# Kernel optimization log

Hardware: AMD Instinct MI355X
Metric: run time of the kernel (lower is better)

Reference implementation:

```python
import jax, jax.numpy as jnp
import numpy as np

B, T, E, H = 2, 2048, 1024, 16
HD = E // H
EPS = 1e-5


def layer_norm(x, g, b):
    mu = jnp.mean(x, axis=-1, keepdims=True)
    var = jnp.mean(jnp.square(x - mu), axis=-1, keepdims=True)
    return (x - mu) * jax.lax.rsqrt(var + EPS) * g + b


def setup_inputs() -> dict:
    key = jax.random.key(0)
    ks = jax.random.split(key, 12)
    s = 0.02
    return {
        "x": jax.random.normal(ks[0], (B, T, E), jnp.float32),
        "Wk": jax.random.normal(ks[1], (E, E), jnp.float32) * s,
        "Wq": jax.random.normal(ks[2], (E, E), jnp.float32) * s,
        "Wv": jax.random.normal(ks[3], (E, E), jnp.float32) * s,
        "Wp": jax.random.normal(ks[4], (E, E), jnp.float32) * s,
        "bp": jnp.zeros((E,), jnp.float32),
        "W1": jax.random.normal(ks[5], (E, 4 * E), jnp.float32) * s,
        "b1": jnp.zeros((4 * E,), jnp.float32),
        "W2": jax.random.normal(ks[6], (4 * E, E), jnp.float32) * s,
        "b2": jnp.zeros((E,), jnp.float32),
        "g1": jnp.ones((E,), jnp.float32),
        "be1": jnp.zeros((E,), jnp.float32),
        "g2": jnp.ones((E,), jnp.float32),
        "be2": jnp.zeros((E,), jnp.float32),
    }


def reference(x, Wk, Wq, Wv, Wp, bp, W1, b1, W2, b2, g1, be1, g2, be2):
    # --- attention sublayer ---
    h = layer_norm(x, g1, be1)
    q = (h @ Wq).reshape(B, T, H, HD).transpose(0, 2, 1, 3)  # [B,H,T,HD]
    k = (h @ Wk).reshape(B, T, H, HD).transpose(0, 2, 1, 3)
    v = (h @ Wv).reshape(B, T, H, HD).transpose(0, 2, 1, 3)
    scores = jnp.einsum('bhqd,bhkd->bhqk', q, k) * (HD ** -0.5)
    causal = jnp.tril(jnp.ones((T, T), bool))
    scores = jnp.where(causal, scores, -jnp.inf)
    probs = jax.nn.softmax(scores, axis=-1)  # dropout is identity (eval)
    attn = jnp.einsum('bhqk,bhkd->bhqd', probs, v)
    attn = attn.transpose(0, 2, 1, 3).reshape(B, T, E)
    x = x + attn @ Wp + bp
    # --- FFN sublayer ---
    h2 = layer_norm(x, g2, be2)
    ff = jax.nn.relu(h2 @ W1 + b1) @ W2 + b2
    return x + ff
```

## Files before the change

### kernel.cpp

```cpp
#include <hip/hip_runtime.h>
#include <hip/hip_bf16.h>

#define B_ 2
#define T_ 2048
#define E_ 1024
#define H_ 16
#define HD_ 64
#define NT (B_*T_)

typedef __attribute__((ext_vector_type(8))) short s16x8;
typedef __attribute__((ext_vector_type(4))) float f32x4;
typedef __attribute__((ext_vector_type(4))) unsigned int u32x4;

using bf16 = __hip_bfloat16;

#define MFMA16(a,b,c) __builtin_amdgcn_mfma_f32_16x16x32_bf16(a,b,c,0,0,0)

__device__ inline unsigned short f2bf(float f) {
    bf16 h = __float2bfloat16(f);
    return *reinterpret_cast<unsigned short*>(&h);
}

__device__ __forceinline__ unsigned cvt_pk_bf16(float lo, float hi) {
    unsigned r;
    asm("v_cvt_pk_bf16_f32 %0, %1, %2" : "=v"(r) : "v"(lo), "v"(hi));
    return r;
}

__device__ __forceinline__ float exp2_fast(float x) {
    float r;
    asm("v_exp_f32 %0, %1" : "=v"(r) : "v"(x));
    return r;
}

__device__ __forceinline__ void async_cp16(const void* g, void* l) {
    __builtin_amdgcn_global_load_lds((const __attribute__((address_space(1))) void*)g,
                                     (__attribute__((address_space(3))) void*)l,
                                     16, 0, 0);
}

__global__ __launch_bounds__(256) void transpose_all(const float* __restrict__ Wq,
                                                     const float* __restrict__ Wk,
                                                     const float* __restrict__ Wv,
                                                     const float* __restrict__ Wp,
                                                     const float* __restrict__ W1,
                                                     const float* __restrict__ W2,
                                                     bf16* __restrict__ Wqkv_t,
                                                     bf16* __restrict__ W1_t,
                                                     bf16* __restrict__ W2_t) {
    __shared__ float tile[32][33];
    int id = blockIdx.x;
    const float* src; bf16* dst; int K, N, n0, k0;
    float scl = 1.0f;
    if (id < 4096) {
        int z = id >> 10, t = id & 1023;
        src = z == 0 ? Wq : z == 1 ? Wk : z == 2 ? Wv : Wp;
        if (z == 0) scl = 0.125f * 1.44269504088896f;
        dst = Wqkv_t + (size_t)z * 1048576;
        K = 1024; N = 1024; n0 = (t & 31) * 32; k0 = (t >> 5) * 32;
    } else if (id < 8192) {
        int t = id - 4096; src = W1; dst = W1_t; K = 1024; N = 4096;
        n0 = (t & 127) * 32; k0 = (t >> 7) * 32;
    } else {
        int t = id - 8192; src = W2; dst = W2_t; K = 4096; N = 1024;
        n0 = (t & 31) * 32; k0 = (t >> 5) * 32;
    }
    int tx = threadIdx.x, ty = threadIdx.y;
#pragma unroll
    for (int i = 0; i < 4; ++i)
        tile[ty + i*8][tx] = src[(size_t)(k0 + ty + i*8)*N + n0 + tx];
    __syncthreads();
#pragma unroll
    for (int i = 0; i < 4; ++i)
        dst[(size_t)(n0 + ty + i*8)*K + k0 + tx] = __float2bfloat16(tile[tx][ty + i*8] * scl);
}

__global__ __launch_bounds__(256) void ln_kernel(const float* __restrict__ x,
                                                 const float* __restrict__ g,
                                                 const float* __restrict__ b,
                                                 bf16* __restrict__ h) {
    int row = blockIdx.x;
    int tid = threadIdx.x;
    const float4 xv = *reinterpret_cast<const float4*>(x + (size_t)row*E_ + tid*4);
    float s  = xv.x + xv.y + xv.z + xv.w;
    float sq = xv.x*xv.x + xv.y*xv.y + xv.z*xv.z + xv.w*xv.w;
#pragma unroll
    for (int o = 32; o > 0; o >>= 1) { s += __shfl_xor(s, o); sq += __shfl_xor(sq, o); }
    __shared__ float red[8];
    int w = tid >> 6, lane = tid & 63;
    if (lane == 0) { red[w] = s; red[4 + w] = sq; }
    __syncthreads();
    float S = red[0] + red[1] + red[2] + red[3];
    float Q = red[4] + red[5] + red[6] + red[7];
    float mu = S * (1.0f/E_);
    float var = Q * (1.0f/E_) - mu*mu;
    float rs = rsqrtf(var + 1e-5f);
    const float4 gv = *reinterpret_cast<const float4*>(g + tid*4);
    const float4 bv = *reinterpret_cast<const float4*>(b + tid*4);
    ushort4 o4;
    o4.x = f2bf((xv.x - mu)*rs*gv.x + bv.x);
    o4.y = f2bf((xv.y - mu)*rs*gv.y + bv.y);
    o4.z = f2bf((xv.z - mu)*rs*gv.z + bv.z);
    o4.w = f2bf((xv.w - mu)*rs*gv.w + bv.w);
    *reinterpret_cast<ushort4*>(h + (size_t)row*E_ + tid*4) = o4;
}

template<int BM, int BN, int EPI>
__global__ __launch_bounds__(256)
void gemm_t(const bf16* __restrict__ A, const bf16* __restrict__ Bt, void* Cout,
            const float* __restrict__ bias, const float* res,
            int M, int N, int K) {
    constexpr int MT = BM / 32;
    constexpr int NB = BN / 32;
    constexpr int MHALF = BM / 2, NHALF = BN / 2;
    __shared__ bf16 As[BM*64];
    __shared__ bf16 Bs[BN*64];
    int tid = threadIdx.x;
    int lane = tid & 63, w = tid >> 6;
    int wr = w >> 1, wc = w & 1;
    int nbx = gridDim.x;
    int hid = blockIdx.y * nbx + blockIdx.x;
    int cpx = (nbx * gridDim.y) >> 3;
    int nid = (hid & 7) * cpx + (hid >> 3);
    int m0 = (nid / nbx) * BM, n0 = (nid % nbx) * BN;
    int lr = lane & 15, lq = lane >> 4;
    f32x4 acc[MT][NB] = {};
    int srow = w*8 + (lane >> 3);
    int schunk = ((lane & 7) ^ (srow & 7)) * 8;
    const bf16* Ap = A  + (size_t)(m0 + srow)*K + schunk;
    const bf16* Bp = Bt + (size_t)(n0 + srow)*K + schunk;
    for (int k0 = 0; k0 < K; k0 += 64) {
#pragma unroll
        for (int i = 0; i < BM/32; ++i)
            async_cp16(Ap + (size_t)(i*32)*K + k0, (char*)As + i*4096 + w*1024);
#pragma unroll
        for (int i = 0; i < BN/32; ++i)
            async_cp16(Bp + (size_t)(i*32)*K + k0, (char*)Bs + i*4096 + w*1024);
        __syncthreads();
        const char* Asb = (const char*)As;
        const char* Bsb = (const char*)Bs;
        s16x8 af[2][MT], bfr[2][NB];
#pragma unroll
        for (int m = 0; m < MT; ++m) {
            int row = wr*MHALF + m*16 + lr;
            int base = row*128, sw = (row & 7) << 4;
#pragma unroll
            for (int kk = 0; kk < 2; ++kk)
                af[kk][m] = *reinterpret_cast<const s16x8*>(Asb + base + ((kk*64 + lq*16) ^ sw));
        }
#pragma unroll
        for (int n = 0; n < NB; ++n) {
            int row = wc*NHALF + n*16 + lr;
            int base = row*128, sw = (row & 7) << 4;
#pragma unroll
            for (int kk = 0; kk < 2; ++kk)
                bfr[kk][n] = *reinterpret_cast<const s16x8*>(Bsb + base + ((kk*64 + lq*16) ^ sw));
        }
        __builtin_amdgcn_s_setprio(1);
#pragma unroll
        for (int kk = 0; kk < 2; ++kk)
#pragma unroll
            for (int m = 0; m < MT; ++m)
#pragma unroll
                for (int n = 0; n < NB; ++n)
                    acc[m][n] = MFMA16(af[kk][m], bfr[kk][n], acc[m][n]);
        __builtin_amdgcn_s_setprio(0);
        __syncthreads();
    }
#pragma unroll
    for (int m = 0; m < MT; ++m) {
#pragma unroll
        for (int n = 0; n < NB; ++n) {
            int col = n0 + wc*NHALF + n*16 + lr;
#pragma unroll
            for (int r = 0; r < 4; ++r) {
                int row = m0 + wr*MHALF + m*16 + lq*4 + r;
                float v = acc[m][n][r];
                if (EPI == 0) {
                    reinterpret_cast<bf16*>(Cout)[(size_t)row*N + col] = __float2bfloat16(v);
                } else if (EPI == 1) {
                    reinterpret_cast<float*>(Cout)[(size_t)row*N + col] =
                        v + bias[col] + res[(size_t)row*N + col];
                } else {
                    v += bias[col];
                    v = v > 0.f ? v : 0.f;
                    reinterpret_cast<bf16*>(Cout)[(size_t)row*N + col] = __float2bfloat16(v);
                }
            }
        }
    }
}

__global__ __launch_bounds__(256) void v_transpose(const bf16* __restrict__ qkv,
                                                   bf16* __restrict__ Vt) {
    __shared__ unsigned short tile[32][33];
    int tx = threadIdx.x, ty = threadIdx.y;
    int bh = blockIdx.z;
    int b = bh >> 4, h = bh & 15;
    int t0 = blockIdx.x * 32, d0 = blockIdx.y * 32;
    const unsigned short* src = reinterpret_cast<const unsigned short*>(qkv);
#pragma unroll
    for (int i = 0; i < 4; ++i)
        tile[ty + i*8][tx] = src[(size_t)(b*T_ + t0 + ty + i*8)*3072 + 2048 + h*64 + d0 + tx];
    __syncthreads();
    unsigned short* dst = reinterpret_cast<unsigned short*>(Vt);
#pragma unroll
    for (int i = 0; i < 4; ++i)
        dst[(size_t)(bh*64 + d0 + ty + i*8)*T_ + t0 + tx] = tile[tx][ty + i*8];
}

__global__ __launch_bounds__(256)
void flash_attn(const bf16* __restrict__ qkv, const bf16* __restrict__ Vt,
                bf16* __restrict__ O) {
    __shared__ char smem[40960];
    int tid = threadIdx.x;
    int lane = tid & 63, w = tid >> 6;
    int lr = lane & 15, lq = lane >> 4;
    int bh = blockIdx.y, b = bh >> 4, h = bh & 15;
    int pm = (bh & 15) ^ ((bh & 16) ? 31 : 0);
    int qt = (int)(blockIdx.x ^ pm) & 31;
    int q0 = qt * 64;
    int qw = q0 + w * 16;
    const bf16* Qb = qkv + (size_t)(b*T_)*3072 + h*HD_;
    const bf16* Kb = Qb + 1024;
    const bf16* Vb = Vt + (size_t)bh * HD_ * T_;
    char* Pw = smem + 32768 + w*2048;

    int srow_ = w*8 + (lane >> 3);
    int sc_   = (((lane & 7) ^ (srow_ & 7))) * 8;
    const bf16* kS0 = Kb + (size_t)srow_*3072 + sc_;
    const bf16* kS1 = kS0 + (size_t)32*3072;
    const bf16* vS0 = Vb + (size_t)srow_*2048 + sc_;
    const bf16* vS1 = vS0 + (size_t)32*2048;
    char* kD = smem + w*1024;
    char* vD = smem + 16384 + w*1024;

    int sw4 = (lr & 7) << 4;
    int kvo[4], pwo[4];
#pragma unroll
    for (int n = 0; n < 4; ++n) {
        kvo[n] = n*2048 + lr*128 + ((lq << 4) ^ sw4);
        pwo[n] = (lr*128 + n*32 + lq*8) ^ sw4;
    }
    int pao0 = (lr*128 + lq*16) ^ sw4;
    int pao1 = (lr*128 + 64 + lq*16) ^ sw4;

    s16x8 qf[2];
#pragma unroll
    for (int kk = 0; kk < 2; ++kk)
        qf[kk] = *reinterpret_cast<const s16x8*>(Qb + (size_t)(qw + lr)*3072 + kk*32 + lq*8);
    f32x4 od[4] = {};
    const f32x4 Z4 = {0.f, 0.f, 0.f, 0.f};
    float lrun = 0.f;
    int ntiles = qt + 1;

    auto stageNext = [&](int bufi) {
        async_cp16(kS0, kD + bufi*8192);
        async_cp16(kS1, kD + bufi*8192 + 4096);
        async_cp16(vS0, vD + bufi*8192);
        async_cp16(vS1, vD + bufi*8192 + 4096);
        kS0 += 64*3072; kS1 += 64*3072; vS0 += 64; vS1 += 64;
    };

    auto step = [&](const char* Kt, const char* Vtl, bool diag, int kv0) {
        f32x4 sc[4];
        __builtin_amdgcn_s_setprio(1);
#pragma unroll
        for (int n = 0; n < 4; ++n) {
            s16x8 kf0 = *reinterpret_cast<const s16x8*>(Kt + kvo[n]);
            s16x8 kf1 = *reinterpret_cast<const s16x8*>(Kt + (kvo[n] ^ 64));
            f32x4 z = MFMA16(kf0, qf[0], Z4);
            z = MFMA16(kf1, qf[1], z);
            sc[n] = z;
        }
        __builtin_amdgcn_s_setprio(0);
        if (diag) {
            int q = qw + lr;
#pragma unroll
            for (int n = 0; n < 4; ++n)
#pragma unroll
                for (int r = 0; r < 4; ++r)
                    if (kv0 + n*16 + lq*4 + r > q) sc[n][r] = -1e30f;
        }
        float psum = 0.f;
#pragma unroll
        for (int n = 0; n < 4; ++n) {
            float p0 = exp2_fast(sc[n][0]);
            float p1 = exp2_fast(sc[n][1]);
            float p2 = exp2_fast(sc[n][2]);
            float p3 = exp2_fast(sc[n][3]);
            psum += (p0 + p1) + (p2 + p3);
            uint2 pk;
            pk.x = cvt_pk_bf16(p0, p1);
            pk.y = cvt_pk_bf16(p2, p3);
            *reinterpret_cast<uint2*>(Pw + pwo[n]) = pk;
        }
        psum += __shfl_xor(psum, 16);
        psum += __shfl_xor(psum, 32);
        lrun += psum;
        asm volatile("" ::: "memory");
        s16x8 pa0 = *reinterpret_cast<const s16x8*>(Pw + pao0);
        s16x8 pa1 = *reinterpret_cast<const s16x8*>(Pw + pao1);
        __builtin_amdgcn_s_setprio(1);
#pragma unroll
        for (int nd = 0; nd < 4; ++nd) {
            s16x8 vf0 = *reinterpret_cast<const s16x8*>(Vtl + kvo[nd]);
            s16x8 vf1 = *reinterpret_cast<const s16x8*>(Vtl + (kvo[nd] ^ 64));
            od[nd] = MFMA16(pa0, vf0, od[nd]);
            od[nd] = MFMA16(pa1, vf1, od[nd]);
        }
        __builtin_amdgcn_s_setprio(0);
    };

    stageNext(0);
    for (int it = 0; it < ntiles - 1; ++it) {
        int curb = it & 1;
        stageNext(curb ^ 1);
        asm volatile("s_waitcnt vmcnt(4)" ::: "memory");
        __builtin_amdgcn_sched_barrier(0);
        __builtin_amdgcn_s_barrier();
        __builtin_amdgcn_sched_barrier(0);
        step(smem + curb*8192, smem + 16384 + curb*8192, false, 0);
        __builtin_amdgcn_sched_barrier(0);
        __builtin_amdgcn_s_barrier();
        __builtin_amdgcn_sched_barrier(0);
    }
    {
        int curb = (ntiles - 1) & 1;
        asm volatile("s_waitcnt vmcnt(0)" ::: "memory");
        __builtin_amdgcn_sched_barrier(0);
        __builtin_amdgcn_s_barrier();
        __builtin_amdgcn_sched_barrier(0);
        step(smem + curb*8192, smem + 16384 + curb*8192, true, (ntiles - 1) * 64);
    }
    float lR[4];
#pragma unroll
    for (int r = 0; r < 4; ++r) lR[r] = 1.0f / __shfl(lrun, lq*4 + r);
#pragma unroll
    for (int nd = 0; nd < 4; ++nd) {
#pragma unroll
        for (int r = 0; r < 4; ++r) {
            int row = qw + lq*4 + r;
            O[(size_t)(b*T_ + row)*E_ + h*HD_ + nd*16 + lr] = __float2bfloat16(od[nd][r] * lR[r]);
        }
    }
}

extern "C" void kernel_launch(void* const* d_in, const int* in_sizes, int n_in,
                              void* d_out, int out_size, void* d_ws, size_t ws_size,
                              hipStream_t stream) {
    const float* x   = (const float*)d_in[0];
    const float* Wk  = (const float*)d_in[1];
    const float* Wq  = (const float*)d_in[2];
    const float* Wv  = (const float*)d_in[3];
    const float* Wp  = (const float*)d_in[4];
    const float* bp  = (const float*)d_in[5];
    const float* W1  = (const float*)d_in[6];
    const float* b1  = (const float*)d_in[7];
    const float* W2  = (const float*)d_in[8];
    const float* b2  = (const float*)d_in[9];
    const float* g1  = (const float*)d_in[10];
    const float* be1 = (const float*)d_in[11];
    const float* g2  = (const float*)d_in[12];
    const float* be2 = (const float*)d_in[13];
    float* out = (float*)d_out;

    char* ws = (char*)d_ws;
    bf16* Wqkv_t = (bf16*)(ws + 0);
    bf16* Wp_t   = (bf16*)(ws + 6291456);
    bf16* W1_t   = (bf16*)(ws + 8388608);
    bf16* W2_t   = (bf16*)(ws + 16777216);
    bf16* h      = (bf16*)(ws + 25165824);
    bf16* qkv    = (bf16*)(ws + 33554432);
    bf16* Vt     = (bf16*)(ws + 58720256);
    bf16* attnO  = (bf16*)(ws + 67108864);
    bf16* ff1    = (bf16*)(ws + 33554432);
    float* x2    = (ws_size >= 92274688) ? (float*)(ws + 75497472) : out;

    dim3 tb(32, 8);
    transpose_all<<<12288, tb, 0, stream>>>(Wq, Wk, Wv, Wp, W1, W2, Wqkv_t, W1_t, W2_t);

    ln_kernel<<<NT, 256, 0, stream>>>(x, g1, be1, h);
    gemm_t<128,128,0><<<dim3(24, 32), 256, 0, stream>>>(h, Wqkv_t, qkv, nullptr, nullptr, NT, 3072, 1024);
    v_transpose<<<dim3(64, 2, 32), tb, 0, stream>>>(qkv, Vt);
    flash_attn<<<dim3(32, 32), 256, 0, stream>>>(qkv, Vt, attnO);
    gemm_t<64,64,1><<<dim3(16, 64), 256, 0, stream>>>(attnO, Wp_t, x2, bp, x, NT, 1024, 1024);
    ln_kernel<<<NT, 256, 0, stream>>>(x2, g2, be2, h);
    gemm_t<128,128,2><<<dim3(32, 32), 256, 0, stream>>>(h, W1_t, ff1, b1, nullptr, NT, 4096, 1024);
    gemm_t<64,64,1><<<dim3(16, 64), 256, 0, stream>>>(ff1, W2_t, out, b2, x2, NT, 1024, 4096);
}
```

Measured before the change: 201.8 us.

## Replace double-buffered K/V staging in flash attention with single-buffer loop

Drops the double-buffered async prefetch of K/V tiles and uses one shared buffer per tile, with __syncthreads before and after each compute step. This cuts LDS use from 40 KB to 24 KB per block, which may allow more resident blocks per CU. In exchange, global-to-LDS copies no longer overlap with MFMA compute inside a block. It also relies on __syncthreads covering completion of the async copies, which the old code enforced with explicit vmcnt waits.

```diff
diff --git a/kernel.cpp b/kernel.cpp
--- a/kernel.cpp
+++ b/kernel.cpp
@@ -212,7 +212,7 @@
 __global__ __launch_bounds__(256)
 void flash_attn(const bf16* __restrict__ qkv, const bf16* __restrict__ Vt,
                 bf16* __restrict__ O) {
-    __shared__ char smem[40960];
+    __shared__ char smem[24576];
     int tid = threadIdx.x;
     int lane = tid & 63, w = tid >> 6;
     int lr = lane & 15, lq = lane >> 4;
@@ -224,7 +224,7 @@
     const bf16* Qb = qkv + (size_t)(b*T_)*3072 + h*HD_;
     const bf16* Kb = Qb + 1024;
     const bf16* Vb = Vt + (size_t)bh * HD_ * T_;
-    char* Pw = smem + 32768 + w*2048;
+    char* Pw = smem + 16384 + w*2048;
 
     int srow_ = w*8 + (lane >> 3);
     int sc_   = (((lane & 7) ^ (srow_ & 7))) * 8;
@@ -233,7 +233,7 @@
     const bf16* vS0 = Vb + (size_t)srow_*2048 + sc_;
     const bf16* vS1 = vS0 + (size_t)32*2048;
     char* kD = smem + w*1024;
-    char* vD = smem + 16384 + w*1024;
+    char* vD = smem + 8192 + w*1024;
 
     int sw4 = (lr & 7) << 4;
     int kvo[4], pwo[4];
@@ -254,15 +254,15 @@
     float lrun = 0.f;
     int ntiles = qt + 1;
 
-    auto stageNext = [&](int bufi) {
-        async_cp16(kS0, kD + bufi*8192);
-        async_cp16(kS1, kD + bufi*8192 + 4096);
-        async_cp16(vS0, vD + bufi*8192);
-        async_cp16(vS1, vD + bufi*8192 + 4096);
+    for (int it = 0; it < ntiles; ++it) {
+        async_cp16(kS0, kD);
+        async_cp16(kS1, kD + 4096);
+        async_cp16(vS0, vD);
+        async_cp16(vS1, vD + 4096);
         kS0 += 64*3072; kS1 += 64*3072; vS0 += 64; vS1 += 64;
-    };
-
-    auto step = [&](const char* Kt, const char* Vtl, bool diag, int kv0) {
+        __syncthreads();
+        const char* Kt = smem;
+        const char* Vtl = smem + 8192;
         f32x4 sc[4];
         __builtin_amdgcn_s_setprio(1);
 #pragma unroll
@@ -274,8 +274,9 @@
             sc[n] = z;
         }
         __builtin_amdgcn_s_setprio(0);
-        if (diag) {
+        if (it == ntiles - 1) {
             int q = qw + lr;
+            int kv0 = it * 64;
 #pragma unroll
             for (int n = 0; n < 4; ++n)
 #pragma unroll
@@ -310,28 +311,7 @@
             od[nd] = MFMA16(pa1, vf1, od[nd]);
         }
         __builtin_amdgcn_s_setprio(0);
-    };
-
-    stageNext(0);
-    for (int it = 0; it < ntiles - 1; ++it) {
-        int curb = it & 1;
-        stageNext(curb ^ 1);
-        asm volatile("s_waitcnt vmcnt(4)" ::: "memory");
-        __builtin_amdgcn_sched_barrier(0);
-        __builtin_amdgcn_s_barrier();
-        __builtin_amdgcn_sched_barrier(0);
-        step(smem + curb*8192, smem + 16384 + curb*8192, false, 0);
-        __builtin_amdgcn_sched_barrier(0);
-        __builtin_amdgcn_s_barrier();
-        __builtin_amdgcn_sched_barrier(0);
-    }
-    {
-        int curb = (ntiles - 1) & 1;
-        asm volatile("s_waitcnt vmcnt(0)" ::: "memory");
-        __builtin_amdgcn_sched_barrier(0);
-        __builtin_amdgcn_s_barrier();
-        __builtin_amdgcn_sched_barrier(0);
-        step(smem + curb*8192, smem + 16384 + curb*8192, true, (ntiles - 1) * 64);
+        __syncthreads();
     }
     float lR[4];
 #pragma unroll
```

New measurement: 204.7 us. No clear change (+1.5%).
